# Kernel tuning notes

Hardware: AMD Instinct MI355X
Metric: run time of the kernel (lower is better)

The kernel has to match this reference:

```python
import jax, jax.numpy as jnp
import numpy as np

DN = ('NCHW', 'OIHW', 'NCHW')
PAD1 = [(1, 1), (1, 1)]


def conv3x3(x, w):
    return jax.lax.conv_general_dilated(x, w, window_strides=(1, 1), padding=PAD1, dimension_numbers=DN)


def setup_inputs() -> dict:
    key = jax.random.key(0)
    ks = jax.random.split(key, 5)
    B, C, H, W = 8, 256, 56, 56
    return {
        'x': jax.random.normal(ks[0], (B, C, H, W), jnp.float32),
        'weight': jax.random.normal(ks[1], (C, C, 3, 3), jnp.float32) * 0.05,
        'A_w': jax.random.normal(ks[2], (1, C, 3, 3), jnp.float32),
        'se_w1': jax.random.normal(ks[3], (16, C, 3, 3), jnp.float32) * 0.02,
        'se_w2': jax.random.normal(ks[4], (1, 16, 3, 3), jnp.float32) * 0.1,
    }


def reference(x, weight, A_w, se_w1, se_w2):
    # weight = weight * A_w (A_w broadcasts over the output-channel dim)
    w = weight * A_w  # [C, C, 3, 3]
    # SE-style spatial attention map A: [B, 1, H, W]
    a = jax.nn.sigmoid(conv3x3(jax.nn.relu(conv3x3(x, se_w1)), se_w2))
    # Torch: unfold(x) * A, then matmul with flattened weight. Since A
    # broadcasts across the C*9 patch dim, this equals conv2d(x, w) * A.
    out = conv3x3(x, w) * a  # [B, C, H, W]
    return out
```

## Files before the change

kernel.cpp:

```cpp
#include <hip/hip_runtime.h>


typedef unsigned short u16;
typedef __bf16 bf16x8 __attribute__((ext_vector_type(8)));
typedef unsigned short us8 __attribute__((ext_vector_type(8)));
typedef float f32x4 __attribute__((ext_vector_type(4)));
typedef float f4v __attribute__((ext_vector_type(4)));

#define HP 58
#define HW 3136

__device__ __forceinline__ u16 f2bf(float f) {
  unsigned u = __float_as_uint(f);
  u = (u + 0x7fffu + ((u >> 16) & 1u)) >> 16;
  return (u16)u;
}
__device__ __forceinline__ float bf2f(u16 v) {
  return __uint_as_float(((unsigned)v) << 16);
}

__device__ __forceinline__ void gload16(const u16* g, u16* l) {
  __builtin_amdgcn_global_load_lds((const __attribute__((address_space(1))) void*)g,
                                   (__attribute__((address_space(3))) void*)l,
                                   16, 0, 0);
}

__global__ void k_prep(const float* __restrict__ weight, const float* __restrict__ A_w,
                       const float* __restrict__ se_w1, u16* __restrict__ wb,
                       u16* __restrict__ w1b) {
  int idx = blockIdx.x * 256 + threadIdx.x;
  if (idx < 589824) {
    int tap = idx >> 16; int rem = idx & 65535; int o = rem >> 8; int c = rem & 255;
    wb[idx] = f2bf(weight[(o * 256 + c) * 9 + tap] * A_w[c * 9 + tap]);
  } else if (idx < 589824 + 36864) {
    int j = idx - 589824;
    int tap = j >> 12; int rem = j & 4095; int o = rem >> 8; int c = rem & 255;
    w1b[j] = f2bf(se_w1[(o * 256 + c) * 9 + tap]);
  }
}

__global__ __launch_bounds__(256) void k_transform(const float* __restrict__ x,
                                                   u16* __restrict__ xp) {
  __shared__ __align__(16) u16 trans[56 * 72];
  const int t = threadIdx.x;
  const int h = blockIdx.x;
  const int b = blockIdx.y;
  for (int cc = 0; cc < 4; ++cc) {
    const int c0 = cc * 64;
#pragma unroll
    for (int i = 0; i < 4; ++i) {
      int idx = t + 256 * i;
      if (idx < 896) {
        int ci = idx / 14, s = idx % 14;
        f4v v = *(const f4v*)(x + ((size_t)(b * 256 + c0 + ci)) * HW + h * 56 + s * 4);
#pragma unroll
        for (int j = 0; j < 4; ++j) trans[(s * 4 + j) * 72 + ci] = f2bf(v[j]);
      }
    }
    __syncthreads();
#pragma unroll
    for (int i = 0; i < 2; ++i) {
      int idx = t + 256 * i;
      if (idx < 448) {
        int w = idx >> 3, seg = idx & 7;
        us8 v = *(const us8*)&trans[w * 72 + seg * 8];
        *(us8*)(xp + ((size_t)((b * HP + h + 1) * HP + (w + 1))) * 256 + c0 + seg * 8) = v;
      }
    }
    __syncthreads();
  }
}

__global__ __launch_bounds__(256) void k_se1(const u16* __restrict__ xp,
                                             const u16* __restrict__ w1b,
                                             float* __restrict__ se1_pre) {
  __shared__ __align__(16) u16 Alds[144 * 72];
  __shared__ __align__(16) u16 Blds[128 * 72];
  const int t = threadIdx.x;
  const int lane = t & 63;
  const int wv = t >> 6;
  const int l15 = lane & 15, lg = lane >> 4;
  const int h0 = blockIdx.x * 2;
  const int b = blockIdx.y;
  const int c0 = blockIdx.z * 64;

  for (int idx = t; idx < 1152; idx += 256) {
    int row = idx >> 3, seg = idx & 7;
    us8 v = *(const us8*)(w1b + ((size_t)row * 256 + c0 + seg * 8));
    *(us8*)&Alds[row * 72 + seg * 8] = v;
  }

  f32x4 acc[2];
  f32x4 z = {0.f, 0.f, 0.f, 0.f};
  acc[0] = z; acc[1] = z;

  for (int dh = 0; dh < 3; ++dh) {
    for (int dw = 0; dw < 3; ++dw) {
      const int tap = dh * 3 + dw;
      __syncthreads();
#pragma unroll
      for (int i = 0; i < 4; ++i) {
        int idx = t + 256 * i;
        int p = idx >> 3, seg = idx & 7;
        int r = p >> 6, w = p & 63, col = w + dw;
        us8 v{};
        if (col < 58)
          v = *(const us8*)(xp + ((size_t)((b * HP + h0 + r + dh) * HP + col)) * 256 + c0 + seg * 8);
        *(us8*)&Blds[p * 72 + seg * 8] = v;
      }
      __syncthreads();
#pragma unroll
      for (int kk = 0; kk < 2; ++kk) {
        bf16x8 af = *(const bf16x8*)&Alds[(tap * 16 + l15) * 72 + kk * 32 + lg * 8];
#pragma unroll
        for (int nt = 0; nt < 2; ++nt) {
          int p = wv * 32 + nt * 16 + l15;
          bf16x8 bfrag = *(const bf16x8*)&Blds[p * 72 + kk * 32 + lg * 8];
          acc[nt] = __builtin_amdgcn_mfma_f32_16x16x32_bf16(af, bfrag, acc[nt], 0, 0, 0);
        }
      }
    }
  }
#pragma unroll
  for (int nt = 0; nt < 2; ++nt) {
    int p = wv * 32 + nt * 16 + l15;
    int r = p >> 6, w = p & 63;
    if (w < 56) {
      int base = ((b * 56 + h0 + r) * 56 + w) * 16 + lg * 4;
#pragma unroll
      for (int reg = 0; reg < 4; ++reg)
        atomicAdd(&se1_pre[base + reg], acc[nt][reg]);
    }
  }
}

__global__ __launch_bounds__(64) void k_se2(const float* __restrict__ se1_pre,
                                            const float* __restrict__ se_w2,
                                            float* __restrict__ amap) {
  __shared__ float w2s[144];
  const int t = threadIdx.x;
  for (int i = t; i < 144; i += 64) w2s[i] = se_w2[i];
  __syncthreads();
  int gid = blockIdx.x * 64 + t;
  int b = gid / HW, p = gid % HW, h = p / 56, w = p % 56;
  float s = 0.f;
  for (int dh = 0; dh < 3; ++dh) {
    int ih = h + dh - 1;
    if (ih < 0 || ih >= 56) continue;
    for (int dw = 0; dw < 3; ++dw) {
      int iw = w + dw - 1;
      if (iw < 0 || iw >= 56) continue;
      const float* src = se1_pre + ((size_t)((b * 56 + ih) * 56 + iw)) * 16;
      int tap = dh * 3 + dw;
#pragma unroll
      for (int c4 = 0; c4 < 4; ++c4) {
        f4v v = *(const f4v*)(src + c4 * 4);
#pragma unroll
        for (int j = 0; j < 4; ++j) {
          float vv = v[j] > 0.f ? v[j] : 0.f;
          s += vv * w2s[(c4 * 4 + j) * 9 + tap];
        }
      }
    }
  }
  amap[gid] = 1.f / (1.f + expf(-s));
}

__global__ __launch_bounds__(256) void k_main(const u16* __restrict__ xp,
                                              const u16* __restrict__ wb,
                                              const float* __restrict__ amap,
                                              float* __restrict__ out) {
  __shared__ __align__(16) u16 Alds[128 * 64];
  __shared__ __align__(16) u16 Blds[128 * 64];
  const int t = threadIdx.x;
  const int lane = t & 63;
  const int wid = t >> 6;
  const int wm = wid >> 1;
  const int wn = wid & 1;
  const int l15 = lane & 15, lg = lane >> 4;
  const int lrow = lane >> 3, lseg = lane & 7;
  const int mbase = blockIdx.x * 128;
  const int h0 = blockIdx.y * 2;
  const int b = blockIdx.z;

  f32x4 acc[4][4];
  f32x4 z = {0.f, 0.f, 0.f, 0.f};
#pragma unroll
  for (int mt = 0; mt < 4; ++mt)
#pragma unroll
    for (int nt = 0; nt < 4; ++nt) acc[mt][nt] = z;

  for (int dh = 0; dh < 3; ++dh) {
    for (int dw = 0; dw < 3; ++dw) {
      const int tap = dh * 3 + dw;
      for (int cc = 0; cc < 4; ++cc) {
        const int c0 = cc * 64;
#pragma unroll
        for (int i = 0; i < 4; ++i) {
          int li = wid * 4 + i;
          int row = li * 8 + lrow;
          const u16* srcA = wb + ((size_t)(tap * 256 + mbase + row)) * 256 + c0 +
                            ((lseg ^ (row & 7)) * 8);
          gload16(srcA, &Alds[li * 512]);
          int r = row >> 6, w = row & 63;
          const u16* srcB = xp +
                            ((size_t)((b * HP + h0 + r + dh) * HP + (w + dw))) * 256 + c0 +
                            ((lseg ^ (row & 7)) * 8);
          gload16(srcB, &Blds[li * 512]);
        }
        __syncthreads();
#pragma unroll
        for (int kk = 0; kk < 2; ++kk) {
          bf16x8 af[4], bfr[4];
#pragma unroll
          for (int mt = 0; mt < 4; ++mt) {
            int row = wm * 64 + mt * 16 + l15;
            af[mt] = *(const bf16x8*)&Alds[row * 64 + (((kk * 4 + lg) ^ (row & 7)) * 8)];
          }
#pragma unroll
          for (int nt = 0; nt < 4; ++nt) {
            int p = wn * 64 + nt * 16 + l15;
            bfr[nt] = *(const bf16x8*)&Blds[p * 64 + (((kk * 4 + lg) ^ (p & 7)) * 8)];
          }
#pragma unroll
          for (int mt = 0; mt < 4; ++mt)
#pragma unroll
            for (int nt = 0; nt < 4; ++nt)
              acc[mt][nt] = __builtin_amdgcn_mfma_f32_16x16x32_bf16(af[mt], bfr[nt], acc[mt][nt], 0, 0, 0);
        }
        __syncthreads();
      }
    }
  }
#pragma unroll
  for (int nt = 0; nt < 4; ++nt) {
    int n = wn * 64 + nt * 16 + l15;
    int r = n >> 6, w = n & 63;
    if (w < 56) {
      float av = amap[(b * 56 + h0 + r) * 56 + w];
#pragma unroll
      for (int mt = 0; mt < 4; ++mt) {
        int obase = mbase + wm * 64 + mt * 16 + lg * 4;
#pragma unroll
        for (int reg = 0; reg < 4; ++reg) {
          out[((size_t)(b * 256 + obase + reg) * 56 + h0 + r) * 56 + w] = acc[mt][nt][reg] * av;
        }
      }
    }
  }
}

extern "C" void kernel_launch(void* const* d_in, const int* in_sizes, int n_in,
                              void* d_out, int out_size, void* d_ws, size_t ws_size,
                              hipStream_t stream) {
  const float* x      = (const float*)d_in[0];
  const float* weight = (const float*)d_in[1];
  const float* A_w    = (const float*)d_in[2];
  const float* se_w1  = (const float*)d_in[3];
  const float* se_w2  = (const float*)d_in[4];
  float* out = (float*)d_out;

  char* ws = (char*)d_ws;
  u16* xp     = (u16*)ws;
  u16* wb     = (u16*)(ws + 13778944);
  u16* w1b    = (u16*)(ws + 14958592);
  float* amap = (float*)(ws + 15032320);
  float* se1_pre = (float*)d_out;

  hipMemsetAsync(xp, 0, 13778944, stream);
  hipMemsetAsync(se1_pre, 0, 1605632, stream);
  k_prep<<<dim3((589824 + 36864 + 255) / 256), dim3(256), 0, stream>>>(weight, A_w, se_w1, wb, w1b);
  k_transform<<<dim3(56, 8), dim3(256), 0, stream>>>(x, xp);
  k_se1<<<dim3(28, 8, 4), dim3(256), 0, stream>>>(xp, w1b, se1_pre);
  k_se2<<<dim3(392), dim3(64), 0, stream>>>(se1_pre, se_w2, amap);
  k_main<<<dim3(2, 28, 8), dim3(256), 0, stream>>>(xp, wb, amap, out);
}
```

Baseline: 172.7 us.

## Double-buffer main conv loads and restructure SE branch without atomics

The main conv kernel now double-buffers its A and B LDS tiles. It issues async global-to-LDS loads for the next tap/channel chunk while the current chunk runs on the MFMAs, with explicit waitcnt and barriers. The SE first conv now loops over all channel chunks inside one block, using a shared input slab reused across the 9 taps, so it no longer needs float atomics. It writes ReLU'd bf16 results into a padded buffer, and the second SE kernel reads those with two threads per pixel and a shuffle reduction. This is meant to hide load latency and remove the atomic and extra memset traffic, at the cost of doubled LDS in k_main and lower SE1 grid parallelism.

```diff
diff --git a/kernel.cpp b/kernel.cpp
--- a/kernel.cpp
+++ b/kernel.cpp
@@ -4,6 +4,7 @@
 typedef unsigned short u16;
 typedef __bf16 bf16x8 __attribute__((ext_vector_type(8)));
 typedef unsigned short us8 __attribute__((ext_vector_type(8)));
+typedef unsigned short us4v __attribute__((ext_vector_type(4)));
 typedef float f32x4 __attribute__((ext_vector_type(4)));
 typedef float f4v __attribute__((ext_vector_type(4)));
 
@@ -73,50 +74,51 @@
 
 __global__ __launch_bounds__(256) void k_se1(const u16* __restrict__ xp,
                                              const u16* __restrict__ w1b,
-                                             float* __restrict__ se1_pre) {
-  __shared__ __align__(16) u16 Alds[144 * 72];
-  __shared__ __align__(16) u16 Blds[128 * 72];
+                                             u16* __restrict__ se1p) {
+  __shared__ __align__(16) u16 Alds[144 * 8 * 8];
+  __shared__ __align__(16) u16 slab[2080 * 8];
   const int t = threadIdx.x;
   const int lane = t & 63;
   const int wv = t >> 6;
   const int l15 = lane & 15, lg = lane >> 4;
   const int h0 = blockIdx.x * 2;
   const int b = blockIdx.y;
-  const int c0 = blockIdx.z * 64;
-
-  for (int idx = t; idx < 1152; idx += 256) {
-    int row = idx >> 3, seg = idx & 7;
-    us8 v = *(const us8*)(w1b + ((size_t)row * 256 + c0 + seg * 8));
-    *(us8*)&Alds[row * 72 + seg * 8] = v;
-  }
 
   f32x4 acc[2];
   f32x4 z = {0.f, 0.f, 0.f, 0.f};
   acc[0] = z; acc[1] = z;
 
-  for (int dh = 0; dh < 3; ++dh) {
-    for (int dw = 0; dw < 3; ++dw) {
-      const int tap = dh * 3 + dw;
-      __syncthreads();
-#pragma unroll
-      for (int i = 0; i < 4; ++i) {
-        int idx = t + 256 * i;
-        int p = idx >> 3, seg = idx & 7;
-        int r = p >> 6, w = p & 63, col = w + dw;
-        us8 v{};
-        if (col < 58)
-          v = *(const us8*)(xp + ((size_t)((b * HP + h0 + r + dh) * HP + col)) * 256 + c0 + seg * 8);
-        *(us8*)&Blds[p * 72 + seg * 8] = v;
-      }
-      __syncthreads();
-#pragma unroll
-      for (int kk = 0; kk < 2; ++kk) {
-        bf16x8 af = *(const bf16x8*)&Alds[(tap * 16 + l15) * 72 + kk * 32 + lg * 8];
-#pragma unroll
-        for (int nt = 0; nt < 2; ++nt) {
-          int p = wv * 32 + nt * 16 + l15;
-          bf16x8 bfrag = *(const bf16x8*)&Blds[p * 72 + kk * 32 + lg * 8];
-          acc[nt] = __builtin_amdgcn_mfma_f32_16x16x32_bf16(af, bfrag, acc[nt], 0, 0, 0);
+  for (int cc = 0; cc < 4; ++cc) {
+    const int c0 = cc * 64;
+    __syncthreads();
+    for (int idx = t; idx < 1152; idx += 256) {
+      int row = idx >> 3, seg = idx & 7;
+      us8 v = *(const us8*)(w1b + ((size_t)row * 256 + c0 + seg * 8));
+      *(us8*)&Alds[(row * 8 + (seg ^ (row & 7))) * 8] = v;
+    }
+#pragma unroll
+    for (int i = 0; i < 8; ++i) {
+      int s_lin = wv * 512 + i * 64 + lane;
+      int r = s_lin >> 9, col = (s_lin >> 3) & 63, seg = s_lin & 7;
+      const u16* src = xp + ((size_t)((b * HP + h0 + r) * HP + col)) * 256 + c0 +
+                       ((seg ^ (col & 7)) * 8);
+      gload16(src, &slab[(wv * 512 + i * 64) * 8]);
+    }
+    __syncthreads();
+    for (int dh = 0; dh < 3; ++dh) {
+      for (int dw = 0; dw < 3; ++dw) {
+        const int tap = dh * 3 + dw;
+#pragma unroll
+        for (int kk = 0; kk < 2; ++kk) {
+          int arow = tap * 16 + l15;
+          bf16x8 af = *(const bf16x8*)&Alds[(arow * 8 + ((kk * 4 + lg) ^ (arow & 7))) * 8];
+#pragma unroll
+          for (int nt = 0; nt < 2; ++nt) {
+            int p = wv * 32 + nt * 16 + l15;
+            int rr = (p >> 6) + dh, col = (p & 63) + dw;
+            bf16x8 bfr = *(const bf16x8*)&slab[((rr * 64 + col) * 8 + ((kk * 4 + lg) ^ (col & 7))) * 8];
+            acc[nt] = __builtin_amdgcn_mfma_f32_16x16x32_bf16(af, bfr, acc[nt], 0, 0, 0);
+          }
         }
       }
     }
@@ -126,52 +128,49 @@
     int p = wv * 32 + nt * 16 + l15;
     int r = p >> 6, w = p & 63;
     if (w < 56) {
-      int base = ((b * 56 + h0 + r) * 56 + w) * 16 + lg * 4;
-#pragma unroll
-      for (int reg = 0; reg < 4; ++reg)
-        atomicAdd(&se1_pre[base + reg], acc[nt][reg]);
-    }
-  }
-}
-
-__global__ __launch_bounds__(64) void k_se2(const float* __restrict__ se1_pre,
-                                            const float* __restrict__ se_w2,
-                                            float* __restrict__ amap) {
+      us4v pk;
+#pragma unroll
+      for (int reg = 0; reg < 4; ++reg) {
+        float v = acc[nt][reg];
+        v = v > 0.f ? v : 0.f;
+        pk[reg] = f2bf(v);
+      }
+      *(us4v*)(se1p + ((size_t)((b * HP + h0 + r + 1) * HP + (w + 1))) * 16 + lg * 4) = pk;
+    }
+  }
+}
+
+__global__ __launch_bounds__(256) void k_se2(const u16* __restrict__ se1p,
+                                             const float* __restrict__ se_w2,
+                                             float* __restrict__ amap) {
   __shared__ float w2s[144];
   const int t = threadIdx.x;
-  for (int i = t; i < 144; i += 64) w2s[i] = se_w2[i];
+  for (int i = t; i < 144; i += 256) w2s[i] = se_w2[i];
   __syncthreads();
-  int gid = blockIdx.x * 64 + t;
-  int b = gid / HW, p = gid % HW, h = p / 56, w = p % 56;
+  int gid = blockIdx.x * 256 + t;
+  int pix = gid >> 1, half = gid & 1;
+  int b = pix / HW, p = pix % HW, h = p / 56, w = p % 56;
   float s = 0.f;
   for (int dh = 0; dh < 3; ++dh) {
-    int ih = h + dh - 1;
-    if (ih < 0 || ih >= 56) continue;
+#pragma unroll
     for (int dw = 0; dw < 3; ++dw) {
-      int iw = w + dw - 1;
-      if (iw < 0 || iw >= 56) continue;
-      const float* src = se1_pre + ((size_t)((b * 56 + ih) * 56 + iw)) * 16;
+      const u16* src = se1p + ((size_t)((b * HP + h + dh) * HP + (w + dw))) * 16 + half * 8;
+      us8 v = *(const us8*)src;
       int tap = dh * 3 + dw;
 #pragma unroll
-      for (int c4 = 0; c4 < 4; ++c4) {
-        f4v v = *(const f4v*)(src + c4 * 4);
-#pragma unroll
-        for (int j = 0; j < 4; ++j) {
-          float vv = v[j] > 0.f ? v[j] : 0.f;
-          s += vv * w2s[(c4 * 4 + j) * 9 + tap];
-        }
-      }
-    }
-  }
-  amap[gid] = 1.f / (1.f + expf(-s));
+      for (int ci = 0; ci < 8; ++ci) s += bf2f(v[ci]) * w2s[(half * 8 + ci) * 9 + tap];
+    }
+  }
+  s += __shfl_xor(s, 1);
+  if (half == 0) amap[pix] = 1.f / (1.f + expf(-s));
 }
 
 __global__ __launch_bounds__(256) void k_main(const u16* __restrict__ xp,
                                               const u16* __restrict__ wb,
                                               const float* __restrict__ amap,
                                               float* __restrict__ out) {
-  __shared__ __align__(16) u16 Alds[128 * 64];
-  __shared__ __align__(16) u16 Blds[128 * 64];
+  __shared__ __align__(16) u16 Alds[2][8192];
+  __shared__ __align__(16) u16 Blds[2][8192];
   const int t = threadIdx.x;
   const int lane = t & 63;
   const int wid = t >> 6;
@@ -190,47 +189,58 @@
 #pragma unroll
     for (int nt = 0; nt < 4; ++nt) acc[mt][nt] = z;
 
-  for (int dh = 0; dh < 3; ++dh) {
-    for (int dw = 0; dw < 3; ++dw) {
-      const int tap = dh * 3 + dw;
-      for (int cc = 0; cc < 4; ++cc) {
-        const int c0 = cc * 64;
-#pragma unroll
-        for (int i = 0; i < 4; ++i) {
-          int li = wid * 4 + i;
-          int row = li * 8 + lrow;
-          const u16* srcA = wb + ((size_t)(tap * 256 + mbase + row)) * 256 + c0 +
-                            ((lseg ^ (row & 7)) * 8);
-          gload16(srcA, &Alds[li * 512]);
-          int r = row >> 6, w = row & 63;
-          const u16* srcB = xp +
-                            ((size_t)((b * HP + h0 + r + dh) * HP + (w + dw))) * 256 + c0 +
-                            ((lseg ^ (row & 7)) * 8);
-          gload16(srcB, &Blds[li * 512]);
-        }
-        __syncthreads();
-#pragma unroll
-        for (int kk = 0; kk < 2; ++kk) {
-          bf16x8 af[4], bfr[4];
-#pragma unroll
-          for (int mt = 0; mt < 4; ++mt) {
-            int row = wm * 64 + mt * 16 + l15;
-            af[mt] = *(const bf16x8*)&Alds[row * 64 + (((kk * 4 + lg) ^ (row & 7)) * 8)];
-          }
-#pragma unroll
-          for (int nt = 0; nt < 4; ++nt) {
-            int p = wn * 64 + nt * 16 + l15;
-            bfr[nt] = *(const bf16x8*)&Blds[p * 64 + (((kk * 4 + lg) ^ (p & 7)) * 8)];
-          }
-#pragma unroll
-          for (int mt = 0; mt < 4; ++mt)
-#pragma unroll
-            for (int nt = 0; nt < 4; ++nt)
-              acc[mt][nt] = __builtin_amdgcn_mfma_f32_16x16x32_bf16(af[mt], bfr[nt], acc[mt][nt], 0, 0, 0);
-        }
-        __syncthreads();
-      }
-    }
+  auto stage = [&](int buf, int it) {
+    const int tap = it >> 2, cc = it & 3;
+    const int dh = tap / 3, dw = tap % 3;
+    const int c0 = cc * 64;
+#pragma unroll
+    for (int i = 0; i < 4; ++i) {
+      int li = wid * 4 + i;
+      int row = li * 8 + lrow;
+      const u16* srcA = wb + ((size_t)(tap * 256 + mbase + row)) * 256 + c0 +
+                        ((lseg ^ (row & 7)) * 8);
+      gload16(srcA, &Alds[buf][li * 512]);
+      int r = row >> 6, w = row & 63;
+      const u16* srcB = xp +
+                        ((size_t)((b * HP + h0 + r + dh) * HP + (w + dw))) * 256 + c0 +
+                        ((lseg ^ (row & 7)) * 8);
+      gload16(srcB, &Blds[buf][li * 512]);
+    }
+  };
+
+  stage(0, 0);
+#pragma unroll 2
+  for (int it = 0; it < 36; ++it) {
+    const int cur = it & 1;
+    if (it < 35) {
+      stage(cur ^ 1, it + 1);
+      asm volatile("s_waitcnt vmcnt(8)" ::: "memory");
+    } else {
+      asm volatile("s_waitcnt vmcnt(0)" ::: "memory");
+    }
+    __builtin_amdgcn_s_barrier();
+    __builtin_amdgcn_sched_barrier(0);
+#pragma unroll
+    for (int kk = 0; kk < 2; ++kk) {
+      bf16x8 af[4], bfr[4];
+#pragma unroll
+      for (int mt = 0; mt < 4; ++mt) {
+        int row = wm * 64 + mt * 16 + l15;
+        af[mt] = *(const bf16x8*)&Alds[cur][row * 64 + (((kk * 4 + lg) ^ (row & 7)) * 8)];
+      }
+#pragma unroll
+      for (int nt = 0; nt < 4; ++nt) {
+        int p = wn * 64 + nt * 16 + l15;
+        bfr[nt] = *(const bf16x8*)&Blds[cur][p * 64 + (((kk * 4 + lg) ^ (p & 7)) * 8)];
+      }
+#pragma unroll
+      for (int mt = 0; mt < 4; ++mt)
+#pragma unroll
+        for (int nt = 0; nt < 4; ++nt)
+          acc[mt][nt] = __builtin_amdgcn_mfma_f32_16x16x32_bf16(af[mt], bfr[nt], acc[mt][nt], 0, 0, 0);
+    }
+    __builtin_amdgcn_sched_barrier(0);
+    __builtin_amdgcn_s_barrier();
   }
 #pragma unroll
   for (int nt = 0; nt < 4; ++nt) {
@@ -262,16 +272,15 @@
 
   char* ws = (char*)d_ws;
   u16* xp     = (u16*)ws;
-  u16* wb     = (u16*)(ws + 13778944);
-  u16* w1b    = (u16*)(ws + 14958592);
-  float* amap = (float*)(ws + 15032320);
-  float* se1_pre = (float*)d_out;
-
-  hipMemsetAsync(xp, 0, 13778944, stream);
-  hipMemsetAsync(se1_pre, 0, 1605632, stream);
+  u16* se1p   = (u16*)(ws + 13778944);
+  u16* wb     = (u16*)(ws + 14640128);
+  u16* w1b    = (u16*)(ws + 15819776);
+  float* amap = (float*)(ws + 15893504);
+
+  hipMemsetAsync(ws, 0, 14640128, stream);
   k_prep<<<dim3((589824 + 36864 + 255) / 256), dim3(256), 0, stream>>>(weight, A_w, se_w1, wb, w1b);
   k_transform<<<dim3(56, 8), dim3(256), 0, stream>>>(x, xp);
-  k_se1<<<dim3(28, 8, 4), dim3(256), 0, stream>>>(xp, w1b, se1_pre);
-  k_se2<<<dim3(392), dim3(64), 0, stream>>>(se1_pre, se_w2, amap);
+  k_se1<<<dim3(28, 8), dim3(256), 0, stream>>>(xp, w1b, se1p);
+  k_se2<<<dim3(196), dim3(256), 0, stream>>>(se1p, se_w2, amap);
   k_main<<<dim3(2, 28, 8), dim3(256), 0, stream>>>(xp, wb, amap, out);
 }
```

Result: faster. 154.3 us (-10.6%).
